# Performance work log

Hardware: AMD Instinct MI355X
Metric: run time of the kernel (lower is better)

## Reference

```python
import jax, jax.numpy as jnp
import numpy as np

H = W = 1024
CHUNK = 32  # rows per chunk in the column EDT pass (keeps intermediate at 32*H*W floats)


def setup_inputs() -> dict:
    key = jax.random.key(0)
    k1, k2 = jax.random.split(key)
    preds = jax.random.randint(k1, (H, W), 0, 2).astype(jnp.float32)
    targets = jax.random.randint(k2, (H, W), 0, 2).astype(jnp.float32)
    return {"preds": preds, "targets": targets}


def _edges(seg):
    # morphological erosion via 3x3 box conv, threshold at 9 == kernel.numel()
    s = seg[None, None]  # (1,1,H,W)
    kern = jnp.ones((1, 1, 3, 3), seg.dtype)
    conv = jax.lax.conv_general_dilated(s, kern, (1, 1), ((1, 1), (1, 1)))
    eroded = (conv[0, 0] == 9.0).astype(seg.dtype)
    return seg - eroded


def _edt(edges):
    # exact Euclidean distance transform: distance to nearest zero of (1 - edges),
    # i.e. nearest pixel where edges == 1.  Separable exact algorithm:
    #   1) per-row 1D distance to nearest feature (via cummax/cummin scans)
    #   2) per-column lower envelope min_k g2[k,j] + (i-k)^2 (chunked brute force)
    feat = (1.0 - edges) == 0.0
    Hh, Ww = edges.shape
    BIG = jnp.float32(1e6)
    col = jnp.arange(Ww, dtype=jnp.float32)
    left = col - jax.lax.cummax(jnp.where(feat, col, -BIG), axis=1)
    right = jax.lax.cummin(jnp.where(feat, col, BIG), axis=1, reverse=True) - col
    g = jnp.minimum(jnp.minimum(left, right), BIG)  # row-wise 1D distance
    g2 = g * g  # (H,W) squared row distances
    rows = jnp.arange(Hh, dtype=jnp.float32)

    def chunk(ic):  # ic: (CHUNK,) target row indices
        # (CHUNK, H, W): g2[k,j] + (i-k)^2, min over source row k
        d = g2[None, :, :] + (ic[:, None, None] - rows[None, :, None]) ** 2
        return jnp.min(d, axis=1)  # (CHUNK, W)

    D2 = jax.lax.map(chunk, rows.reshape(-1, CHUNK)).reshape(Hh, Ww)
    return jnp.sqrt(D2)


def reference(preds, targets):
    pred_edges = _edges(preds)
    target_edges = _edges(targets)
    # scipy EDT ran on detached CPU copies -> no gradient through the DTs
    pred_dt = jax.lax.stop_gradient(_edt(pred_edges))
    target_dt = jax.lax.stop_gradient(_edt(target_edges))
    pred_err = target_edges * pred_dt
    target_err = pred_edges * target_dt
    loss = (jnp.mean(pred_err) + jnp.mean(target_err)) / 2.0
    return jax.nn.sigmoid(loss)
```

## Files before the change

kernel.cpp:

```cpp
#include <hip/hip_runtime.h>
#include <math.h>


#define HW 1024
#define BIGF 1e6f
#define RMIN_SENT (1 << 30)

__global__ __launch_bounds__(256)
void k_rows(const float* __restrict__ pred, const float* __restrict__ targ,
            float* __restrict__ hp, float* __restrict__ ht,
            unsigned char* __restrict__ ep, unsigned char* __restrict__ et)
{
    const int t    = threadIdx.x;
    const int lane = t & 63;
    const int wv   = t >> 6;
    const int r    = blockIdx.x * 4 + wv;
    const int m    = blockIdx.y;
    const float* __restrict__ seg = m ? targ : pred;
    float* __restrict__ hout = m ? ht : hp;
    unsigned char* __restrict__ eout = m ? et : ep;

    const int c0 = lane * 16;

    float cs[16], cm[16], cp[16];
    #pragma unroll
    for (int q = 0; q < 4; ++q)
        *(float4*)&cs[q * 4] = *(const float4*)&seg[r * HW + c0 + q * 4];
    #pragma unroll
    for (int q = 0; q < 4; ++q) {
        *(float4*)&cm[q * 4] = make_float4(0.f, 0.f, 0.f, 0.f);
        *(float4*)&cp[q * 4] = make_float4(0.f, 0.f, 0.f, 0.f);
    }
    if (r > 0) {
        #pragma unroll
        for (int q = 0; q < 4; ++q)
            *(float4*)&cm[q * 4] = *(const float4*)&seg[(r - 1) * HW + c0 + q * 4];
    }
    if (r < HW - 1) {
        #pragma unroll
        for (int q = 0; q < 4; ++q)
            *(float4*)&cp[q * 4] = *(const float4*)&seg[(r + 1) * HW + c0 + q * 4];
    }

    unsigned s_bits = 0, va_bits = 0;
    #pragma unroll
    for (int x = 0; x < 16; ++x) {
        const unsigned s  = (cs[x] != 0.f) ? 1u : 0u;
        const unsigned va = (cs[x] != 0.f && cm[x] != 0.f && cp[x] != 0.f) ? 1u : 0u;
        s_bits  |= s  << x;
        va_bits |= va << x;
    }

    const unsigned vprev = __shfl_up(va_bits, 1);
    const unsigned vnext = __shfl_down(va_bits, 1);
    const unsigned lbit = (lane == 0)  ? 0u : ((vprev >> 15) & 1u);
    const unsigned rbit = (lane == 63) ? 0u : (vnext & 1u);

    const unsigned w18 = (va_bits << 1) | lbit | (rbit << 17);
    const unsigned eroded = w18 & (w18 >> 1) & (w18 >> 2);
    const unsigned edge = s_bits & ~eroded & 0xFFFFu;

    uint4 eb;
    unsigned ew[4];
    #pragma unroll
    for (int q = 0; q < 4; ++q) {
        unsigned u = 0;
        #pragma unroll
        for (int b = 0; b < 4; ++b)
            u |= ((edge >> (q * 4 + b)) & 1u) << (8 * b);
        ew[q] = u;
    }
    eb.x = ew[0]; eb.y = ew[1]; eb.z = ew[2]; eb.w = ew[3];
    *(uint4*)&eout[r * HW + c0] = eb;

    const int lane_last  = edge ? (c0 + 31 - __clz(edge)) : -1;
    const int lane_first = edge ? (c0 + __ffs(edge) - 1)  : RMIN_SENT;

    int Li = lane_last;
    #pragma unroll
    for (int off = 1; off < 64; off <<= 1) {
        const int v = __shfl_up(Li, off);
        if (lane >= off) Li = max(Li, v);
    }
    int Ri = lane_first;
    #pragma unroll
    for (int off = 1; off < 64; off <<= 1) {
        const int v = __shfl_down(Ri, off);
        if (lane + off < 64) Ri = min(Ri, v);
    }
    int carryL = __shfl_up(Li, 1);   if (lane == 0)  carryL = -1;
    int carryR = __shfl_down(Ri, 1); if (lane == 63) carryR = RMIN_SENT;

    const float rr = (float)(r * r);
    float hv[16];
    #pragma unroll
    for (int x = 0; x < 16; ++x) {
        const unsigned ble = edge & ((2u << x) - 1u);
        const int L = ble ? (c0 + 31 - __clz(ble)) : carryL;
        const unsigned bge = edge >> x;
        const int R = bge ? (c0 + x + __ffs(bge) - 1) : carryR;
        const float jf = (float)(c0 + x);
        const float left  = jf - ((L < 0) ? -BIGF : (float)L);
        const float right = ((R >= RMIN_SENT) ? BIGF : (float)R) - jf;
        const float g = fminf(fminf(left, right), BIGF);
        hv[x] = g * g + rr;
    }
    #pragma unroll
    for (int q = 0; q < 4; ++q)
        *(float4*)&hout[r * HW + c0 + q * 4] = *(float4*)&hv[q * 4];
}

#define WIN 8
#define RPB 128
#define KROWS (RPB + 2 * WIN)
#define HS_STRIDE 17

__global__ __launch_bounds__(256)
void k_cols(const float* __restrict__ hp, const float* __restrict__ ht,
            const unsigned char* __restrict__ ep, const unsigned char* __restrict__ et,
            float* __restrict__ partial)
{
    const int j0 = blockIdx.x * 16;
    const int i0 = blockIdx.y * RPB;
    const int m  = blockIdx.z;
    const float* __restrict__ hg = m ? ht : hp;
    const unsigned char* __restrict__ ew = m ? ep : et;

    __shared__ float hs[KROWS * HS_STRIDE];
    __shared__ alignas(16) unsigned char es[RPB * 16];
    __shared__ float wsum[4];

    for (int idx = threadIdx.x; idx < KROWS * 16; idx += 256) {
        const int kk = idx >> 4, jc = idx & 15;
        const int gk = i0 - WIN + kk;
        float v = 1e30f;
        if ((unsigned)gk < (unsigned)HW) v = hg[gk * HW + j0 + jc];
        hs[kk * HS_STRIDE + jc] = v;
    }
    if (threadIdx.x < RPB)
        *(uint4*)&es[threadIdx.x * 16] = *(const uint4*)&ew[(i0 + threadIdx.x) * HW + j0];
    __syncthreads();

    const int jj = threadIdx.x & 15;
    const int iw = threadIdx.x >> 4;
    float lsum = 0.f;

    #pragma unroll
    for (int g = 0; g < 2; ++g) {
        const int ib = i0 + iw * 8 + g * 4;
        const int kkS = iw * 8 + g * 4;
        float b0 = 3e38f, b1 = 3e38f, b2 = 3e38f, b3 = 3e38f;
        float kf = (float)(ib - WIN);
        const float m0 = -2.f * (float)(ib);
        const float m1 = -2.f * (float)(ib + 1);
        const float m2 = -2.f * (float)(ib + 2);
        const float m3 = -2.f * (float)(ib + 3);
        #pragma unroll
        for (int kk = kkS; kk < kkS + 2 * WIN + 4; ++kk) {
            const float hvv = hs[kk * HS_STRIDE + jj];
            b0 = fminf(b0, fmaf(m0, kf, hvv));
            b1 = fminf(b1, fmaf(m1, kf, hvv));
            b2 = fminf(b2, fmaf(m2, kf, hvv));
            b3 = fminf(b3, fmaf(m3, kf, hvv));
            kf += 1.f;
        }
        const int sLo = max(0, ib - WIN);
        const int sHi = min(HW - 1, ib + WIN + 3);
        float bs[4] = {b0, b1, b2, b3};
        #pragma unroll
        for (int w = 0; w < 4; ++w) {
            const int i = ib + w;
            float D2 = (float)(i * i) + bs[w];
            const int dl = i - sLo + 1, dr = sHi + 1 - i;
            const bool need = ((sLo > 0) && (D2 > (float)(dl * dl))) ||
                              ((sHi < HW - 1) && (D2 > (float)(dr * dr)));
            if (need) {
                float bb = 3e38f, k2 = 0.f;
                const float mm = -2.f * (float)i;
                for (int k = 0; k < HW; ++k) {
                    bb = fminf(bb, fmaf(mm, k2, hg[k * HW + j0 + jj]));
                    k2 += 1.f;
                }
                D2 = (float)(i * i) + bb;
            }
            const float wgt = (float)es[(i - i0) * 16 + jj];
            lsum = fmaf(wgt, sqrtf(D2), lsum);
        }
    }

    #pragma unroll
    for (int off = 32; off > 0; off >>= 1) lsum += __shfl_down(lsum, off);
    if ((threadIdx.x & 63) == 0) wsum[threadIdx.x >> 6] = lsum;
    __syncthreads();
    if (threadIdx.x == 0) {
        const int bid = blockIdx.x + 64 * (blockIdx.y + 8 * blockIdx.z);
        partial[bid] = wsum[0] + wsum[1] + wsum[2] + wsum[3];
    }
}

__global__ __launch_bounds__(256)
void k_fin(const float* __restrict__ partial, float* __restrict__ out)
{
    const int t = threadIdx.x;
    float s = partial[t] + partial[t + 256] + partial[t + 512] + partial[t + 768];
    #pragma unroll
    for (int off = 32; off > 0; off >>= 1) s += __shfl_down(s, off);
    __shared__ float w[4];
    if ((t & 63) == 0) w[t >> 6] = s;
    __syncthreads();
    if (t == 0) {
        const float tot = w[0] + w[1] + w[2] + w[3];
        const float loss = tot * (1.f / (2.f * 1024.f * 1024.f));
        out[0] = 1.f / (1.f + expf(-loss));
    }
}

extern "C" void kernel_launch(void* const* d_in, const int* in_sizes, int n_in,
                              void* d_out, int out_size, void* d_ws, size_t ws_size,
                              hipStream_t stream)
{
    const float* preds   = (const float*)d_in[0];
    const float* targets = (const float*)d_in[1];
    float* out = (float*)d_out;

    char* ws = (char*)d_ws;
    float* hp = (float*)ws;
    float* ht = hp + HW * HW;
    unsigned char* ep = (unsigned char*)(ht + HW * HW);
    unsigned char* et = ep + HW * HW;
    float* partial = (float*)(et + HW * HW);

    dim3 gA(HW / 4, 2, 1);
    k_rows<<<gA, 256, 0, stream>>>(preds, targets, hp, ht, ep, et);

    dim3 gB(HW / 16, HW / RPB, 2);
    k_cols<<<gB, 256, 0, stream>>>(hp, ht, ep, et, partial);

    k_fin<<<1, 256, 0, stream>>>(partial, out);
}
```

Before: 77.13 us.

## Compress row distances to u16, bit-pack edges, fuse final reduction via atomics

The row pass now stores the 1D distance to the nearest edge as a 16-bit integer instead of a float squared distance plus r², and stores edge masks as 16-bit bitfields in a column-major layout instead of one byte per pixel. The column pass rebuilds g²+k² on load. The separate finalize kernel is removed: the last k_cols block, found through a two-level atomic counter, sums the partials and writes the sigmoid. This cuts intermediate memory traffic and one launch, at the cost of extra conversion arithmetic, a fence, atomics, and a slower fallback full-column loop.

```diff
diff --git a/kernel.cpp b/kernel.cpp
--- a/kernel.cpp
+++ b/kernel.cpp
@@ -3,13 +3,17 @@
 
 
 #define HW 1024
-#define BIGF 1e6f
 #define RMIN_SENT (1 << 30)
+#define WIN 8
+#define RPB 128
+#define KROWS (RPB + 2 * WIN)
+#define HS_STRIDE 17
 
 __global__ __launch_bounds__(256)
 void k_rows(const float* __restrict__ pred, const float* __restrict__ targ,
-            float* __restrict__ hp, float* __restrict__ ht,
-            unsigned char* __restrict__ ep, unsigned char* __restrict__ et)
+            unsigned short* __restrict__ gp, unsigned short* __restrict__ gt,
+            unsigned short* __restrict__ epb, unsigned short* __restrict__ etb,
+            unsigned* __restrict__ cnts)
 {
     const int t    = threadIdx.x;
     const int lane = t & 63;
@@ -17,8 +21,10 @@
     const int r    = blockIdx.x * 4 + wv;
     const int m    = blockIdx.y;
     const float* __restrict__ seg = m ? targ : pred;
-    float* __restrict__ hout = m ? ht : hp;
-    unsigned char* __restrict__ eout = m ? et : ep;
+    unsigned short* __restrict__ gout = m ? gt : gp;
+    unsigned short* __restrict__ ebout = m ? etb : epb;
+
+    if (blockIdx.x == 0 && m == 0 && t < 17) cnts[t] = 0u;
 
     const int c0 = lane * 16;
 
@@ -60,18 +66,7 @@
     const unsigned eroded = w18 & (w18 >> 1) & (w18 >> 2);
     const unsigned edge = s_bits & ~eroded & 0xFFFFu;
 
-    uint4 eb;
-    unsigned ew[4];
-    #pragma unroll
-    for (int q = 0; q < 4; ++q) {
-        unsigned u = 0;
-        #pragma unroll
-        for (int b = 0; b < 4; ++b)
-            u |= ((edge >> (q * 4 + b)) & 1u) << (8 * b);
-        ew[q] = u;
-    }
-    eb.x = ew[0]; eb.y = ew[1]; eb.z = ew[2]; eb.w = ew[3];
-    *(uint4*)&eout[r * HW + c0] = eb;
+    ebout[lane * HW + r] = (unsigned short)edge;
 
     const int lane_last  = edge ? (c0 + 31 - __clz(edge)) : -1;
     const int lane_first = edge ? (c0 + __ffs(edge) - 1)  : RMIN_SENT;
@@ -91,54 +86,62 @@
     int carryL = __shfl_up(Li, 1);   if (lane == 0)  carryL = -1;
     int carryR = __shfl_down(Ri, 1); if (lane == 63) carryR = RMIN_SENT;
 
-    const float rr = (float)(r * r);
-    float hv[16];
+    unsigned short gv[16];
     #pragma unroll
     for (int x = 0; x < 16; ++x) {
         const unsigned ble = edge & ((2u << x) - 1u);
         const int L = ble ? (c0 + 31 - __clz(ble)) : carryL;
         const unsigned bge = edge >> x;
         const int R = bge ? (c0 + x + __ffs(bge) - 1) : carryR;
-        const float jf = (float)(c0 + x);
-        const float left  = jf - ((L < 0) ? -BIGF : (float)L);
-        const float right = ((R >= RMIN_SENT) ? BIGF : (float)R) - jf;
-        const float g = fminf(fminf(left, right), BIGF);
-        hv[x] = g * g + rr;
-    }
-    #pragma unroll
-    for (int q = 0; q < 4; ++q)
-        *(float4*)&hout[r * HW + c0 + q * 4] = *(float4*)&hv[q * 4];
+        const int j = c0 + x;
+        int g;
+        if (L < 0 && R >= RMIN_SENT)      g = 65535;
+        else if (L < 0)                   g = R - j;
+        else if (R >= RMIN_SENT)          g = j - L;
+        else                              g = min(j - L, R - j);
+        gv[x] = (unsigned short)g;
+    }
+    unsigned wpk[8];
+    #pragma unroll
+    for (int k2 = 0; k2 < 8; ++k2)
+        wpk[k2] = (unsigned)gv[2 * k2] | ((unsigned)gv[2 * k2 + 1] << 16);
+    uint4 st0, st1;
+    st0.x = wpk[0]; st0.y = wpk[1]; st0.z = wpk[2]; st0.w = wpk[3];
+    st1.x = wpk[4]; st1.y = wpk[5]; st1.z = wpk[6]; st1.w = wpk[7];
+    *(uint4*)&gout[r * HW + c0]     = st0;
+    *(uint4*)&gout[r * HW + c0 + 8] = st1;
 }
 
-#define WIN 8
-#define RPB 128
-#define KROWS (RPB + 2 * WIN)
-#define HS_STRIDE 17
-
 __global__ __launch_bounds__(256)
-void k_cols(const float* __restrict__ hp, const float* __restrict__ ht,
-            const unsigned char* __restrict__ ep, const unsigned char* __restrict__ et,
-            float* __restrict__ partial)
+void k_cols(const unsigned short* __restrict__ gp, const unsigned short* __restrict__ gt,
+            const unsigned short* __restrict__ epb, const unsigned short* __restrict__ etb,
+            float* __restrict__ partial, unsigned* __restrict__ cnts,
+            float* __restrict__ out)
 {
     const int j0 = blockIdx.x * 16;
     const int i0 = blockIdx.y * RPB;
     const int m  = blockIdx.z;
-    const float* __restrict__ hg = m ? ht : hp;
-    const unsigned char* __restrict__ ew = m ? ep : et;
+    const unsigned short* __restrict__ gg = m ? gt : gp;
+    const unsigned short* __restrict__ ewb = m ? epb : etb;
 
     __shared__ float hs[KROWS * HS_STRIDE];
-    __shared__ alignas(16) unsigned char es[RPB * 16];
+    __shared__ unsigned short esb[RPB];
     __shared__ float wsum[4];
+    __shared__ int winf;
 
     for (int idx = threadIdx.x; idx < KROWS * 16; idx += 256) {
         const int kk = idx >> 4, jc = idx & 15;
         const int gk = i0 - WIN + kk;
         float v = 1e30f;
-        if ((unsigned)gk < (unsigned)HW) v = hg[gk * HW + j0 + jc];
+        if ((unsigned)gk < (unsigned)HW) {
+            const unsigned gu = gg[gk * HW + j0 + jc];
+            float gf = (gu == 65535u) ? (1e6f - (float)(j0 + jc)) : (float)gu;
+            v = fmaf(gf, gf, (float)(gk * gk));
+        }
         hs[kk * HS_STRIDE + jc] = v;
     }
     if (threadIdx.x < RPB)
-        *(uint4*)&es[threadIdx.x * 16] = *(const uint4*)&ew[(i0 + threadIdx.x) * HW + j0];
+        esb[threadIdx.x] = ewb[(j0 >> 4) * HW + i0 + threadIdx.x];
     __syncthreads();
 
     const int jj = threadIdx.x & 15;
@@ -178,13 +181,16 @@
                 float bb = 3e38f, k2 = 0.f;
                 const float mm = -2.f * (float)i;
                 for (int k = 0; k < HW; ++k) {
-                    bb = fminf(bb, fmaf(mm, k2, hg[k * HW + j0 + jj]));
+                    const unsigned gu = gg[k * HW + j0 + jj];
+                    const float gf = (gu == 65535u) ? (1e6f - (float)(j0 + jj))
+                                                    : (float)gu;
+                    bb = fminf(bb, fmaf(mm, k2, fmaf(gf, gf, k2 * k2)));
                     k2 += 1.f;
                 }
                 D2 = (float)(i * i) + bb;
             }
-            const float wgt = (float)es[(i - i0) * 16 + jj];
-            lsum = fmaf(wgt, sqrtf(D2), lsum);
+            const unsigned wbit = (esb[i - i0] >> jj) & 1u;
+            lsum += wbit ? sqrtf(D2) : 0.f;
         }
     }
 
@@ -192,26 +198,34 @@
     for (int off = 32; off > 0; off >>= 1) lsum += __shfl_down(lsum, off);
     if ((threadIdx.x & 63) == 0) wsum[threadIdx.x >> 6] = lsum;
     __syncthreads();
+
+    const int bid = blockIdx.x + 64 * (blockIdx.y + 8 * blockIdx.z);
     if (threadIdx.x == 0) {
-        const int bid = blockIdx.x + 64 * (blockIdx.y + 8 * blockIdx.z);
         partial[bid] = wsum[0] + wsum[1] + wsum[2] + wsum[3];
-    }
-}
-
-__global__ __launch_bounds__(256)
-void k_fin(const float* __restrict__ partial, float* __restrict__ out)
-{
-    const int t = threadIdx.x;
-    float s = partial[t] + partial[t + 256] + partial[t + 512] + partial[t + 768];
-    #pragma unroll
-    for (int off = 32; off > 0; off >>= 1) s += __shfl_down(s, off);
-    __shared__ float w[4];
-    if ((t & 63) == 0) w[t >> 6] = s;
+        __threadfence();
+        int w = 0;
+        const unsigned v = atomicAdd(&cnts[bid & 15], 1u);
+        if (v == 63u) {
+            const unsigned v2 = atomicAdd(&cnts[16], 1u);
+            if (v2 == 15u) w = 1;
+        }
+        winf = w;
+    }
     __syncthreads();
-    if (t == 0) {
-        const float tot = w[0] + w[1] + w[2] + w[3];
-        const float loss = tot * (1.f / (2.f * 1024.f * 1024.f));
-        out[0] = 1.f / (1.f + expf(-loss));
+
+    if (winf) {
+        __threadfence();
+        const int t = threadIdx.x;
+        float s = partial[t] + partial[t + 256] + partial[t + 512] + partial[t + 768];
+        #pragma unroll
+        for (int off = 32; off > 0; off >>= 1) s += __shfl_down(s, off);
+        if ((t & 63) == 0) wsum[t >> 6] = s;
+        __syncthreads();
+        if (t == 0) {
+            const float tot = wsum[0] + wsum[1] + wsum[2] + wsum[3];
+            const float loss = tot * (1.f / (2.f * 1024.f * 1024.f));
+            out[0] = 1.f / (1.f + expf(-loss));
+        }
     }
 }
 
@@ -224,17 +238,16 @@
     float* out = (float*)d_out;
 
     char* ws = (char*)d_ws;
-    float* hp = (float*)ws;
-    float* ht = hp + HW * HW;
-    unsigned char* ep = (unsigned char*)(ht + HW * HW);
-    unsigned char* et = ep + HW * HW;
-    float* partial = (float*)(et + HW * HW);
+    unsigned short* gp  = (unsigned short*)ws;
+    unsigned short* gt  = gp + HW * HW;
+    unsigned short* epb = gt + HW * HW;
+    unsigned short* etb = epb + 64 * HW;
+    float* partial = (float*)(etb + 64 * HW);
+    unsigned* cnts = (unsigned*)(partial + 1024);
 
     dim3 gA(HW / 4, 2, 1);
-    k_rows<<<gA, 256, 0, stream>>>(preds, targets, hp, ht, ep, et);
+    k_rows<<<gA, 256, 0, stream>>>(preds, targets, gp, gt, epb, etb, cnts);
 
     dim3 gB(HW / 16, HW / RPB, 2);
-    k_cols<<<gB, 256, 0, stream>>>(hp, ht, ep, et, partial);
-
-    k_fin<<<1, 256, 0, stream>>>(partial, out);
+    k_cols<<<gB, 256, 0, stream>>>(gp, gt, epb, etb, partial, cnts, out);
 }
```

Result: slower. 91.49 us (+18.6%).
